# Kernel tuning notes

Hardware: AMD Instinct MI355X
Metric: run time of the kernel (lower is better)

The kernel has to match this reference:

```python
import jax, jax.numpy as jnp
import numpy as np

LEVEL_NUM = 8  # init kwarg level_num (scale is unused by forward)


def setup_inputs() -> dict:
    key = jax.random.key(0)
    x = jax.random.normal(key, (1, 1024, 1024), dtype=jnp.float32)
    return {"x": x}


def reference(x):
    N, H, W = x.shape
    L = LEVEL_NUM
    q_levels = jnp.linspace(x.min(), x.max(), L)          # (L,)
    sigma = 2.0 / L                                        # 1 / (level_num/2)
    # soft quantization: (N,H,W,L)
    quant = jnp.exp(-((x[..., None] - q_levels) ** 2) / (sigma ** 2))
    quant = jnp.transpose(quant, (0, 3, 1, 2))             # (N,L,H,W)
    quant = jnp.pad(quant, ((0, 0), (0, 0), (0, 1), (0, 1)))  # (N,L,H+1,W+1)
    quant_left = quant[:, :, None, :H, :W]                 # (N,L,1,H,W)
    quant_right = quant[:, None, :, 1:, 1:]                # (N,1,L,H,W)
    co_occurrence = quant_left * quant_right               # (N,L,L,H,W)
    sta = co_occurrence.sum(axis=(-1, -2))                 # (N,L,L)
    sta = sta / sta.sum(axis=(1, 2))                       # valid since N==1
    # q_levels_h[n,i,j] = q_levels[j]; q_levels_w[n,i,j] = q_levels[i]
    q_h = jnp.broadcast_to(q_levels[None, None, :], (N, L, L))
    q_w = jnp.broadcast_to(q_levels[None, :, None], (N, L, L))
    output = jnp.stack([q_h, q_w, sta], axis=1).reshape(N, 3, L * L)[0]  # (3, L*L)
    return output, quant[0], co_occurrence[0]
```

## Files before the change

kernel.cpp:

```cpp
#include <hip/hip_runtime.h>

#define H 1024
#define W 1024
#define L 8
#define QH 1025
#define QW 1025
#define OUT0 192
#define QUANT_ELEMS (L * QH * QW)

#define WS_MIN 0
#define WS_MAX 16
#define WS_STA 32
#define WS_STRIDE 16
#define WS_SLOTS (WS_STA + 64 * WS_STRIDE)

__device__ __forceinline__ unsigned enc_ord(float f) {
    unsigned b = __float_as_uint(f);
    return (b & 0x80000000u) ? ~b : (b ^ 0x80000000u);
}
__device__ __forceinline__ float dec_ord(unsigned u) {
    unsigned b = (u & 0x80000000u) ? (u ^ 0x80000000u) : ~u;
    return __uint_as_float(b);
}

__global__ void k_init(unsigned* ws) {
    int t = threadIdx.x;
    for (int i = t; i < WS_SLOTS; i += 256)
        ws[i] = (i == WS_MIN) ? 0xFFFFFFFFu : 0u;
}

__global__ __launch_bounds__(256) void k_minmax(const float4* __restrict__ x4, unsigned* ws) {
    int t = threadIdx.x;
    int gid = blockIdx.x * 256 + t;
    float mn = 1e30f, mx = -1e30f;
    #pragma unroll
    for (int i = 0; i < 4; ++i) {
        float4 v = x4[gid + i * 65536];
        mn = fminf(mn, fminf(fminf(v.x, v.y), fminf(v.z, v.w)));
        mx = fmaxf(mx, fmaxf(fmaxf(v.x, v.y), fmaxf(v.z, v.w)));
    }
    #pragma unroll
    for (int m = 1; m < 64; m <<= 1) {
        mn = fminf(mn, __shfl_xor(mn, m, 64));
        mx = fmaxf(mx, __shfl_xor(mx, m, 64));
    }
    __shared__ float smn[4], smx[4];
    if ((t & 63) == 0) { smn[t >> 6] = mn; smx[t >> 6] = mx; }
    __syncthreads();
    if (t == 0) {
        mn = fminf(fminf(smn[0], smn[1]), fminf(smn[2], smn[3]));
        mx = fmaxf(fmaxf(smx[0], smx[1]), fmaxf(smx[2], smx[3]));
        atomicMin(&ws[WS_MIN], enc_ord(mn));
        atomicMax(&ws[WS_MAX], enc_ord(mx));
    }
}

__global__ __launch_bounds__(256) void k_main(const float* __restrict__ x,
                                              float* __restrict__ out,
                                              unsigned* __restrict__ ws) {
    const float mnv = dec_ord(ws[WS_MIN]);
    const float mxv = dec_ord(ws[WS_MAX]);
    const float step = (mxv - mnv) * (1.0f / 7.0f);
    float q[L];
    #pragma unroll
    for (int i = 0; i < L; ++i) q[i] = mnv + step * (float)i;
    q[L - 1] = mxv;

    float* __restrict__ quant = out + OUT0;
    float* __restrict__ co    = out + OUT0 + QUANT_ELEMS;

    const int t = threadIdx.x, h = blockIdx.x;
    const int w0 = t * 4, lane = t & 63, wv = t >> 6;

    float4 xl = *(const float4*)(x + h * W + w0);
    float xls[4] = {xl.x, xl.y, xl.z, xl.w};

    const bool hok = (h + 1 < H);
    float rv[4][L];
    #pragma unroll
    for (int p = 0; p < 4; ++p) {
        int rw = w0 + 1 + p;
        bool ok = hok && (rw < W);
        float xr = ok ? x[(h + 1) * W + rw] : 0.0f;
        #pragma unroll
        for (int j = 0; j < L; ++j) {
            float d = xr - q[j];
            rv[p][j] = ok ? __expf(-16.0f * d * d) : 0.0f;
        }
    }

    float acc[64];
    #pragma unroll
    for (int i = 0; i < L; ++i) {
        float lv[4];
        #pragma unroll
        for (int p = 0; p < 4; ++p) {
            float d = xls[p] - q[i];
            lv[p] = __expf(-16.0f * d * d);
        }
        float* qp = quant + (i * QH + h) * QW + w0;
        qp[0] = lv[0]; qp[1] = lv[1]; qp[2] = lv[2]; qp[3] = lv[3];

        #pragma unroll
        for (int j = 0; j < L; ++j) {
            float4 v;
            v.x = lv[0] * rv[0][j];
            v.y = lv[1] * rv[1][j];
            v.z = lv[2] * rv[2][j];
            v.w = lv[3] * rv[3][j];
            *(float4*)(co + ((i * L + j) * H + h) * W + w0) = v;
            acc[i * L + j] = (v.x + v.y) + (v.z + v.w);
        }
    }

    if (t < L) quant[(t * QH + h) * QW + W] = 0.0f;
    if (h < L) {
        for (int w = t; w < QW; w += 256) quant[(h * QH + H) * QW + w] = 0.0f;
    }

    int cnt = 64;
    #pragma unroll
    for (int s = 0; s < 6; ++s) {
        const int m = 1 << s;
        const int half = cnt >> 1;
        const bool upper = (lane & m) != 0;
        #pragma unroll
        for (int k = 0; k < half; ++k) {
            float a = acc[k], b = acc[k + half];
            float keep = upper ? b : a;
            float send = upper ? a : b;
            float recv = __shfl_xor(send, m, 64);
            acc[k] = keep + recv;
        }
        cnt = half;
    }
    const int col = __brev(lane) >> 26;

    __shared__ float red[4][64];
    red[wv][col] = acc[0];
    __syncthreads();
    if (t < 64) {
        float s4 = (red[0][t] + red[1][t]) + (red[2][t] + red[3][t]);
        atomicAdd((float*)ws + WS_STA + t * WS_STRIDE, s4);
    }
}

__global__ void k_final(float* __restrict__ out, const unsigned* __restrict__ ws) {
    int t = threadIdx.x;
    const float mnv = dec_ord(ws[WS_MIN]);
    const float mxv = dec_ord(ws[WS_MAX]);
    const float step = (mxv - mnv) * (1.0f / 7.0f);
    float q[L];
    #pragma unroll
    for (int i = 0; i < L; ++i) q[i] = mnv + step * (float)i;
    q[L - 1] = mxv;

    float s = ((const float*)ws)[WS_STA + t * WS_STRIDE];
    float tot = s;
    #pragma unroll
    for (int m = 1; m < 64; m <<= 1) tot += __shfl_xor(tot, m, 64);

    out[t]       = q[t & 7];
    out[64 + t]  = q[t >> 3];
    out[128 + t] = s / tot;
}

extern "C" void kernel_launch(void* const* d_in, const int* in_sizes, int n_in,
                              void* d_out, int out_size, void* d_ws, size_t ws_size,
                              hipStream_t stream) {
    const float* x = (const float*)d_in[0];
    float* out = (float*)d_out;
    unsigned* ws = (unsigned*)d_ws;

    k_init<<<dim3(1), dim3(256), 0, stream>>>(ws);
    k_minmax<<<dim3(256), dim3(256), 0, stream>>>((const float4*)x, ws);
    k_main<<<dim3(H), dim3(256), 0, stream>>>(x, out, ws);
    k_final<<<dim3(1), dim3(64), 0, stream>>>(out, ws);
}
```

Measured before the change: 75.53 us.

## Split main kernel by co-occurrence pair and row chunk to cut register pressure

After: 72.81 us. 3.6% less time.

```diff
diff --git a/kernel.cpp b/kernel.cpp
--- a/kernel.cpp
+++ b/kernel.cpp
@@ -7,6 +7,10 @@
 #define QW 1025
 #define OUT0 192
 #define QUANT_ELEMS (L * QH * QW)
+
+#define CROWS 32
+#define NCHUNK 32
+#define BPC 72
 
 #define WS_MIN 0
 #define WS_MAX 16
@@ -21,6 +25,9 @@
 __device__ __forceinline__ float dec_ord(unsigned u) {
     unsigned b = (u & 0x80000000u) ? (u ^ 0x80000000u) : ~u;
     return __uint_as_float(b);
+}
+__device__ __forceinline__ float qlev(float mn, float step, float mx, int i) {
+    return (i == L - 1) ? mx : mn + step * (float)i;
 }
 
 __global__ void k_init(unsigned* ws) {
@@ -61,87 +68,78 @@
     const float mnv = dec_ord(ws[WS_MIN]);
     const float mxv = dec_ord(ws[WS_MAX]);
     const float step = (mxv - mnv) * (1.0f / 7.0f);
-    float q[L];
-    #pragma unroll
-    for (int i = 0; i < L; ++i) q[i] = mnv + step * (float)i;
-    q[L - 1] = mxv;
 
     float* __restrict__ quant = out + OUT0;
     float* __restrict__ co    = out + OUT0 + QUANT_ELEMS;
 
-    const int t = threadIdx.x, h = blockIdx.x;
-    const int w0 = t * 4, lane = t & 63, wv = t >> 6;
+    const int bid = blockIdx.x;
+    const int c = bid / BPC, k = bid - c * BPC;
+    const int r0 = c * CROWS;
+    const int t = threadIdx.x, w0 = t * 4;
 
-    float4 xl = *(const float4*)(x + h * W + w0);
-    float xls[4] = {xl.x, xl.y, xl.z, xl.w};
+    if (k < 64) {
+        const int i = k >> 3, j = k & 7;
+        const float qi = qlev(mnv, step, mxv, i);
+        const float qj = qlev(mnv, step, mxv, j);
+        float* cop = co + k * (H * W) + r0 * W + w0;
+        float acc = 0.0f;
 
-    const bool hok = (h + 1 < H);
-    float rv[4][L];
-    #pragma unroll
-    for (int p = 0; p < 4; ++p) {
-        int rw = w0 + 1 + p;
-        bool ok = hok && (rw < W);
-        float xr = ok ? x[(h + 1) * W + rw] : 0.0f;
-        #pragma unroll
-        for (int j = 0; j < L; ++j) {
-            float d = xr - q[j];
-            rv[p][j] = ok ? __expf(-16.0f * d * d) : 0.0f;
+        for (int r = 0; r < CROWS; ++r) {
+            const int h = r0 + r;
+            float4 xl = *(const float4*)(x + h * W + w0);
+            const bool hok = (h + 1 < H);
+            float xr0 = 0.f, xr1 = 0.f, xr2 = 0.f, xr3 = 0.f;
+            bool ok3 = false;
+            if (hok) {
+                float4 a = *(const float4*)(x + (h + 1) * W + w0);
+                xr0 = a.y; xr1 = a.z; xr2 = a.w;
+                ok3 = (w0 + 4 < W);
+                if (ok3) xr3 = x[(h + 1) * W + w0 + 4];
+            }
+            float d;
+            d = xl.x - qi; float l0 = __expf(-16.f * d * d);
+            d = xl.y - qi; float l1 = __expf(-16.f * d * d);
+            d = xl.z - qi; float l2 = __expf(-16.f * d * d);
+            d = xl.w - qi; float l3 = __expf(-16.f * d * d);
+            d = xr0 - qj; float p0 = hok ? __expf(-16.f * d * d) : 0.f;
+            d = xr1 - qj; float p1 = hok ? __expf(-16.f * d * d) : 0.f;
+            d = xr2 - qj; float p2 = hok ? __expf(-16.f * d * d) : 0.f;
+            d = xr3 - qj; float p3 = (hok && ok3) ? __expf(-16.f * d * d) : 0.f;
+
+            float4 v;
+            v.x = l0 * p0; v.y = l1 * p1; v.z = l2 * p2; v.w = l3 * p3;
+            *(float4*)cop = v;
+            cop += W;
+            acc += (v.x + v.y) + (v.z + v.w);
         }
-    }
-
-    float acc[64];
-    #pragma unroll
-    for (int i = 0; i < L; ++i) {
-        float lv[4];
-        #pragma unroll
-        for (int p = 0; p < 4; ++p) {
-            float d = xls[p] - q[i];
-            lv[p] = __expf(-16.0f * d * d);
-        }
-        float* qp = quant + (i * QH + h) * QW + w0;
-        qp[0] = lv[0]; qp[1] = lv[1]; qp[2] = lv[2]; qp[3] = lv[3];
 
         #pragma unroll
-        for (int j = 0; j < L; ++j) {
-            float4 v;
-            v.x = lv[0] * rv[0][j];
-            v.y = lv[1] * rv[1][j];
-            v.z = lv[2] * rv[2][j];
-            v.w = lv[3] * rv[3][j];
-            *(float4*)(co + ((i * L + j) * H + h) * W + w0) = v;
-            acc[i * L + j] = (v.x + v.y) + (v.z + v.w);
+        for (int m = 1; m < 64; m <<= 1) acc += __shfl_xor(acc, m, 64);
+        __shared__ float red[4];
+        if ((t & 63) == 0) red[t >> 6] = acc;
+        __syncthreads();
+        if (t == 0)
+            atomicAdd((float*)ws + WS_STA + k * WS_STRIDE,
+                      (red[0] + red[1]) + (red[2] + red[3]));
+    } else {
+        const int i = k - 64;
+        const float qi = qlev(mnv, step, mxv, i);
+        for (int r = 0; r < CROWS; ++r) {
+            const int h = r0 + r;
+            float4 xl = *(const float4*)(x + h * W + w0);
+            float d;
+            d = xl.x - qi; float l0 = __expf(-16.f * d * d);
+            d = xl.y - qi; float l1 = __expf(-16.f * d * d);
+            d = xl.z - qi; float l2 = __expf(-16.f * d * d);
+            d = xl.w - qi; float l3 = __expf(-16.f * d * d);
+            float* row = quant + (i * QH + h) * QW + w0;
+            row[0] = l0; row[1] = l1; row[2] = l2; row[3] = l3;
+            if (t == 255) row[4] = 0.0f;
         }
-    }
-
-    if (t < L) quant[(t * QH + h) * QW + W] = 0.0f;
-    if (h < L) {
-        for (int w = t; w < QW; w += 256) quant[(h * QH + H) * QW + w] = 0.0f;
-    }
-
-    int cnt = 64;
-    #pragma unroll
-    for (int s = 0; s < 6; ++s) {
-        const int m = 1 << s;
-        const int half = cnt >> 1;
-        const bool upper = (lane & m) != 0;
-        #pragma unroll
-        for (int k = 0; k < half; ++k) {
-            float a = acc[k], b = acc[k + half];
-            float keep = upper ? b : a;
-            float send = upper ? a : b;
-            float recv = __shfl_xor(send, m, 64);
-            acc[k] = keep + recv;
+        if (c == NCHUNK - 1) {
+            for (int w = t; w < QW; w += 256)
+                quant[(i * QH + H) * QW + w] = 0.0f;
         }
-        cnt = half;
-    }
-    const int col = __brev(lane) >> 26;
-
-    __shared__ float red[4][64];
-    red[wv][col] = acc[0];
-    __syncthreads();
-    if (t < 64) {
-        float s4 = (red[0][t] + red[1][t]) + (red[2][t] + red[3][t]);
-        atomicAdd((float*)ws + WS_STA + t * WS_STRIDE, s4);
     }
 }
 
@@ -150,18 +148,14 @@
     const float mnv = dec_ord(ws[WS_MIN]);
     const float mxv = dec_ord(ws[WS_MAX]);
     const float step = (mxv - mnv) * (1.0f / 7.0f);
-    float q[L];
-    #pragma unroll
-    for (int i = 0; i < L; ++i) q[i] = mnv + step * (float)i;
-    q[L - 1] = mxv;
 
     float s = ((const float*)ws)[WS_STA + t * WS_STRIDE];
     float tot = s;
     #pragma unroll
     for (int m = 1; m < 64; m <<= 1) tot += __shfl_xor(tot, m, 64);
 
-    out[t]       = q[t & 7];
-    out[64 + t]  = q[t >> 3];
+    out[t]       = qlev(mnv, step, mxv, t & 7);
+    out[64 + t]  = qlev(mnv, step, mxv, t >> 3);
     out[128 + t] = s / tot;
 }
 
@@ -174,6 +168,6 @@
 
     k_init<<<dim3(1), dim3(256), 0, stream>>>(ws);
     k_minmax<<<dim3(256), dim3(256), 0, stream>>>((const float4*)x, ws);
-    k_main<<<dim3(H), dim3(256), 0, stream>>>(x, out, ws);
+    k_main<<<dim3(NCHUNK * BPC), dim3(256), 0, stream>>>(x, out, ws);
     k_final<<<dim3(1), dim3(64), 0, stream>>>(out, ws);
 }
```
